# Optimization experiments

Measured on AMD Instinct MI355X. Metric: run time of the kernel, lower is better.

## Reference

```python
import jax, jax.numpy as jnp
import numpy as np

DIM = 1024
D_INNER = 2048

def setup_inputs() -> dict:
    key = jax.random.key(0)
    ks = jax.random.split(key, 8)
    B, T = 8, 1024
    x = jax.random.normal(ks[0], (B, T, DIM), dtype=jnp.float32)
    h0 = jnp.zeros((B, D_INNER), dtype=jnp.float32)
    # params (xavier-ish scales)
    in_proj_w = jax.random.normal(ks[1], (D_INNER, DIM), dtype=jnp.float32) * (2.0 / (DIM + D_INNER)) ** 0.5
    out_proj_w = jax.random.normal(ks[2], (DIM, D_INNER), dtype=jnp.float32) * (2.0 / (DIM + D_INNER)) ** 0.5
    c_h = jax.random.uniform(ks[3], (D_INNER,), jnp.float32, -0.1, 0.1)
    # spectral normalization as in _init_weights
    c_h = c_h * jnp.minimum(1.0, 0.99 / jnp.abs(jnp.fft.fft(c_h)).max())
    c_x = jax.random.uniform(ks[4], (D_INNER,), jnp.float32, -0.1, 0.1)
    c_x = c_x * jnp.minimum(1.0, 0.99 / jnp.abs(jnp.fft.fft(c_x)).max())
    b = jnp.zeros((D_INNER,), dtype=jnp.float32)
    W_gate = jax.random.normal(ks[5], (D_INNER, D_INNER), dtype=jnp.float32) * (1.0 / D_INNER) ** 0.5
    b_gate = jnp.zeros((D_INNER,), dtype=jnp.float32)
    return {"x": x, "h0": h0, "in_proj_w": in_proj_w, "out_proj_w": out_proj_w,
            "c_h": c_h, "c_x": c_x, "b": b, "W_gate": W_gate, "b_gate": b_gate}

def _circ_apply_fft(fft_c, v):
    # circ(c) @ v along last axis via real FFT; v: [..., D]
    D = v.shape[-1]
    return jnp.fft.irfft(fft_c * jnp.fft.rfft(v, axis=-1), n=D, axis=-1)

def reference(x, h0, in_proj_w, out_proj_w, c_h, c_x, b, W_gate, b_gate):
    B, T, _ = x.shape
    D = h0.shape[-1]
    x_proj = jnp.einsum('btd,ed->bte', x, in_proj_w)  # [B,T,D_inner]
    # gate path (fully parallel over T)
    gate = jax.nn.silu(jnp.einsum('bte,fe->btf', x_proj, W_gate) + b_gate)
    # input circulant contribution, parallel over all tokens
    pre = _circ_apply_fft(jnp.fft.rfft(c_x), x_proj) + b  # [B,T,D]
    fft_ch = jnp.fft.rfft(c_h)

    def step(h_prev, pre_t):
        h_new = jnp.tanh(_circ_apply_fft(fft_ch, h_prev) + pre_t)
        return h_new, h_new

    pre_tbd = jnp.transpose(pre, (1, 0, 2))  # [T,B,D]
    h_final, h_seq = jax.lax.scan(step, h0, pre_tbd)  # h_seq: [T,B,D]
    cell_out = jnp.transpose(h_seq, (1, 0, 2)) * gate  # [B,T,D]
    output = jnp.einsum('bte,de->btd', cell_out, out_proj_w)  # [B,T,dim]
    return output, h_final
```

## Files before the change

### kernel.cpp

```cpp
#include <hip/hip_runtime.h>
#include <cstdint>
#include <cstddef>

#define DI 2048
#define DM 1024
#define BB 8
#define TT 1024
#define ROWS (BB*TT)

typedef short  short8 __attribute__((ext_vector_type(8)));
typedef float  f32x4  __attribute__((ext_vector_type(4)));
typedef float  f32x16 __attribute__((ext_vector_type(16)));

__device__ __forceinline__ unsigned short f2bf(float f) {
  unsigned int u = __builtin_bit_cast(unsigned int, f);
  u = u + 0x7fffu + ((u >> 16) & 1u);
  return (unsigned short)(u >> 16);
}
__device__ __forceinline__ float fast_tanh(float x) {
  float ax = fabsf(x);
  float e  = __expf(-2.0f * ax);
  float t  = (1.0f - e) / (1.0f + e);
  return x < 0.0f ? -t : t;
}
__device__ __forceinline__ float silu_f(float z) {
  return z / (1.0f + __expf(-z));
}
__device__ __forceinline__ unsigned mulpk(unsigned a, unsigned b) {
  float a0 = __builtin_bit_cast(float, a << 16);
  float a1 = __builtin_bit_cast(float, a & 0xffff0000u);
  float b0 = __builtin_bit_cast(float, b << 16);
  float b1 = __builtin_bit_cast(float, b & 0xffff0000u);
  unsigned r0 = f2bf(a0 * b0), r1 = f2bf(a1 * b1);
  return r0 | (r1 << 16);
}
__device__ __forceinline__ uint4 pack8(const unsigned short* q) {
  uint4 p;
  p.x = (unsigned)q[0] | ((unsigned)q[1] << 16);
  p.y = (unsigned)q[2] | ((unsigned)q[3] << 16);
  p.z = (unsigned)q[4] | ((unsigned)q[5] << 16);
  p.w = (unsigned)q[6] | ((unsigned)q[7] << 16);
  return p;
}

__global__ void cast_k(const float* __restrict__ s, short* __restrict__ d, int n4) {
  int i = blockIdx.x * 256 + threadIdx.x;
  if (i >= n4) return;
  float4 f = ((const float4*)s)[i];
  unsigned lo = (unsigned)f2bf(f.x) | ((unsigned)f2bf(f.y) << 16);
  unsigned hi = (unsigned)f2bf(f.z) | ((unsigned)f2bf(f.w) << 16);
  uint2 o; o.x = lo; o.y = hi;
  ((uint2*)d)[i] = o;
}

__global__ void build_cx_k(const float* __restrict__ cx, short* __restrict__ C) {
  int tid = blockIdx.x * 256 + threadIdx.x;
  int n   = tid >> 8;
  int k0  = (tid & 255) * 8;
  unsigned short q[8];
#pragma unroll
  for (int j = 0; j < 8; ++j) q[j] = f2bf(cx[(n - (k0 + j)) & (DI - 1)]);
  *(uint4*)(C + (size_t)n * DI + k0) = pack8(q);
}

__global__ __launch_bounds__(256) void gemm_k(
    const short* __restrict__ A, const short* __restrict__ A2,
    const short* __restrict__ Bt,
    int M, int N, int K, int mode, const float* __restrict__ bias,
    float* __restrict__ outF, short* __restrict__ outH)
{
  __shared__ __align__(16) short As[128 * 40];
  __shared__ __align__(16) short Bs[128 * 40];
  const int tid  = threadIdx.x;
  const int m0   = blockIdx.y * 128, n0 = blockIdx.x * 128;
  const int wave = tid >> 6, lane = tid & 63;
  const int wy = wave >> 1, wx = wave & 1;
  const int l = lane & 15, G = lane >> 4;
  const int srow = tid >> 1, sseg = tid & 1;

  f32x4 acc[4][4];
#pragma unroll
  for (int i = 0; i < 4; ++i)
#pragma unroll
    for (int j = 0; j < 4; ++j) acc[i][j] = (f32x4){0.f, 0.f, 0.f, 0.f};

  for (int k0 = 0; k0 < K; k0 += 32) {
    if (k0) __syncthreads();
    const short* ga = A  + (size_t)(m0 + srow) * K + k0 + sseg * 16;
    const short* gb = Bt + (size_t)(n0 + srow) * K + k0 + sseg * 16;
    uint4 a0 = *(const uint4*)ga;
    uint4 a1 = *(const uint4*)(ga + 8);
    if (A2) {
      const short* g2 = A2 + (size_t)(m0 + srow) * K + k0 + sseg * 16;
      uint4 m0v = *(const uint4*)g2;
      uint4 m1v = *(const uint4*)(g2 + 8);
      a0.x = mulpk(a0.x, m0v.x); a0.y = mulpk(a0.y, m0v.y);
      a0.z = mulpk(a0.z, m0v.z); a0.w = mulpk(a0.w, m0v.w);
      a1.x = mulpk(a1.x, m1v.x); a1.y = mulpk(a1.y, m1v.y);
      a1.z = mulpk(a1.z, m1v.z); a1.w = mulpk(a1.w, m1v.w);
    }
    uint4 b0 = *(const uint4*)gb;
    uint4 b1 = *(const uint4*)(gb + 8);
    *(uint4*)&As[srow * 40 + sseg * 16]     = a0;
    *(uint4*)&As[srow * 40 + sseg * 16 + 8] = a1;
    *(uint4*)&Bs[srow * 40 + sseg * 16]     = b0;
    *(uint4*)&Bs[srow * 40 + sseg * 16 + 8] = b1;
    __syncthreads();
    short8 af[4], bfv[4];
#pragma unroll
    for (int i = 0; i < 4; ++i) af[i]  = *(const short8*)&As[(64 * wy + 16 * i + l) * 40 + 8 * G];
#pragma unroll
    for (int j = 0; j < 4; ++j) bfv[j] = *(const short8*)&Bs[(64 * wx + 16 * j + l) * 40 + 8 * G];
#pragma unroll
    for (int i = 0; i < 4; ++i)
#pragma unroll
      for (int j = 0; j < 4; ++j)
        acc[i][j] = __builtin_amdgcn_mfma_f32_16x16x32_bf16(af[i], bfv[j], acc[i][j], 0, 0, 0);
  }

#pragma unroll
  for (int j = 0; j < 4; ++j) {
    const int c = n0 + 64 * wx + 16 * j + l;
    float bv = 0.f;
    if (mode == 1 || mode == 2) bv = bias[c];
#pragma unroll
    for (int i = 0; i < 4; ++i) {
      const int r0 = m0 + 64 * wy + 16 * i + 4 * G;
#pragma unroll
      for (int v = 0; v < 4; ++v) {
        float z = acc[i][j][v] + bv;
        size_t off = (size_t)(r0 + v) * N + c;
        if (mode == 0)      outH[off] = (short)f2bf(z);
        else if (mode == 2) outH[off] = (short)f2bf(silu_f(z));
        else                outF[off] = z;
      }
    }
  }
}

__global__ __launch_bounds__(512, 2) void fused_k(
    const float* __restrict__ pre, const float* __restrict__ h0,
    const float* __restrict__ ch, short* __restrict__ hseq,
    float* __restrict__ hfin,
    const short* __restrict__ xproj, const short* __restrict__ wg,
    const float* __restrict__ bg, short* __restrict__ gate)
{
  __shared__ __align__(16) char smem[53248];
  const int bid = blockIdx.x;
  const int tid = threadIdx.x;

  if (bid < BB) {
    short* h_lds   = (short*)smem;
    float* pre_lds = (float*)(smem + 4096);
    float* part    = (float*)(smem + 20480);
    const int b = bid;
    const int wid = tid >> 6, lane = tid & 63;
    const int nh = wid & 1, kg = wid >> 1;
    const int L = lane & 31, G2 = lane >> 5;
    const int q = 32 * nh + L;
    const float* preB = pre + (size_t)b * TT * DI;

    short8 av[32];
#pragma unroll
    for (int i = 0; i < 32; ++i) {
      const int kbase = 16 * (32 * kg + i) + 8 * G2;
      short8 v;
#pragma unroll
      for (int j = 0; j < 8; ++j)
        v[j] = (short)f2bf(ch[(L - kbase - j) & (DI - 1)]);
      av[i] = v;
    }

    {
      const int n0 = 4 * tid;
      float4 hv = *(const float4*)(h0 + b * DI + n0);
      unsigned lo = (unsigned)f2bf(hv.x) | ((unsigned)f2bf(hv.y) << 16);
      unsigned hi = (unsigned)f2bf(hv.z) | ((unsigned)f2bf(hv.w) << 16);
      const int blk = tid >> 1;
      const int pblk = blk ^ ((blk >> 3) & 7);
      uint2 w; w.x = lo; w.y = hi;
      *(uint2*)&h_lds[pblk * 8 + 4 * (tid & 1)] = w;
      *(float4*)&pre_lds[n0] = *(const float4*)(preB + n0);
    }
    __syncthreads();

    const int cbase = (G2 + 4 * q + 64 * kg) & 255;

    for (int t = 0; t < TT; ++t) {
      const int cur = t & 1;
      const float* pn = preB + (size_t)(t + 1 < TT ? t + 1 : t) * DI;
      float4 pf = *(const float4*)(pn + 4 * tid);

      f32x16 acc0, acc1;
#pragma unroll
      for (int v = 0; v < 16; ++v) { acc0[v] = 0.f; acc1[v] = 0.f; }
#pragma unroll
      for (int i = 0; i < 32; i += 2) {
        int blkA = (cbase + 2 * i) & 255;
        int blkB = (cbase + 2 * i + 2) & 255;
        int pA = blkA ^ ((blkA >> 3) & 7);
        int pB = blkB ^ ((blkB >> 3) & 7);
        short8 bvA = *(const short8*)&h_lds[pA * 8];
        short8 bvB = *(const short8*)&h_lds[pB * 8];
        acc0 = __builtin_amdgcn_mfma_f32_32x32x16_bf16(av[i],     bvA, acc0, 0, 0, 0);
        acc1 = __builtin_amdgcn_mfma_f32_32x32x16_bf16(av[i + 1], bvB, acc1, 0, 0, 0);
      }
      {
        float* pk = part + kg * DI;
#pragma unroll
        for (int s = 0; s < 4; ++s) {
          const int blk4 = 2 * s + G2 + 8 * q;
          const int p4 = blk4 ^ ((blk4 >> 3) & 7);
          float4 w;
          w.x = acc0[4 * s + 0] + acc1[4 * s + 0];
          w.y = acc0[4 * s + 1] + acc1[4 * s + 1];
          w.z = acc0[4 * s + 2] + acc1[4 * s + 2];
          w.w = acc0[4 * s + 3] + acc1[4 * s + 3];
          *(float4*)&pk[4 * p4] = w;
        }
        *(float4*)&pre_lds[(cur ^ 1) * DI + 4 * tid] = pf;
      }
      __syncthreads();
      {
        const int pb = tid ^ ((tid >> 3) & 7);
        float4 c0 = *(const float4*)&part[4 * pb];
        float4 c1 = *(const float4*)&part[DI + 4 * pb];
        float4 c2 = *(const float4*)&part[2 * DI + 4 * pb];
        float4 c3 = *(const float4*)&part[3 * DI + 4 * pb];
        float4 pr = *(const float4*)&pre_lds[cur * DI + 4 * tid];
        float z0 = c0.x + c1.x + c2.x + c3.x + pr.x;
        float z1 = c0.y + c1.y + c2.y + c3.y + pr.y;
        float z2 = c0.z + c1.z + c2.z + c3.z + pr.z;
        float z3 = c0.w + c1.w + c2.w + c3.w + pr.w;
        float t0 = fast_tanh(z0), t1 = fast_tanh(z1);
        float t2 = fast_tanh(z2), t3 = fast_tanh(z3);
        unsigned lo = (unsigned)f2bf(t0) | ((unsigned)f2bf(t1) << 16);
        unsigned hi = (unsigned)f2bf(t2) | ((unsigned)f2bf(t3) << 16);
        const int blk = tid >> 1;
        const int pblk = blk ^ ((blk >> 3) & 7);
        uint2 w; w.x = lo; w.y = hi;
        *(uint2*)&h_lds[pblk * 8 + 4 * (tid & 1)] = w;
        *(uint2*)(hseq + (size_t)(b * TT + t) * DI + 4 * tid) = w;
        if (t == TT - 1) {
          float4 hf; hf.x = t0; hf.y = t1; hf.z = t2; hf.w = t3;
          *(float4*)(hfin + b * DI + 4 * tid) = hf;
        }
      }
      __syncthreads();
    }
  } else {
    short* As = (short*)smem;
    short* Bs = (short*)(smem + 20480);
    const int wid = tid >> 6, lane = tid & 63;
    const int wy = wid >> 1, wx = wid & 1;
    const int l = lane & 15, G = lane >> 4;

    for (int tile = bid - BB; tile < 512; tile += 248) {
      const int m0 = (tile & 31) * 256, n0 = (tile >> 5) * 128;
      f32x4 acc[4][4];
#pragma unroll
      for (int i = 0; i < 4; ++i)
#pragma unroll
        for (int j = 0; j < 4; ++j) acc[i][j] = (f32x4){0.f, 0.f, 0.f, 0.f};

      for (int k0 = 0; k0 < DI; k0 += 32) {
        __syncthreads();
        const short* ga = xproj + (size_t)(m0 + (tid >> 1)) * DI + k0 + (tid & 1) * 16;
        const short* gb = wg    + (size_t)(n0 + (tid >> 2)) * DI + k0 + (tid & 3) * 8;
        uint4 a0 = *(const uint4*)ga;
        uint4 a1 = *(const uint4*)(ga + 8);
        uint4 b0 = *(const uint4*)gb;
        *(uint4*)&As[(tid >> 1) * 40 + (tid & 1) * 16]     = a0;
        *(uint4*)&As[(tid >> 1) * 40 + (tid & 1) * 16 + 8] = a1;
        *(uint4*)&Bs[(tid >> 2) * 40 + (tid & 3) * 8]      = b0;
        __syncthreads();
        short8 af[4], bfv[4];
#pragma unroll
        for (int i = 0; i < 4; ++i) af[i]  = *(const short8*)&As[(64 * wy + 16 * i + l) * 40 + 8 * G];
#pragma unroll
        for (int j = 0; j < 4; ++j) bfv[j] = *(const short8*)&Bs[(64 * wx + 16 * j + l) * 40 + 8 * G];
#pragma unroll
        for (int i = 0; i < 4; ++i)
#pragma unroll
          for (int j = 0; j < 4; ++j)
            acc[i][j] = __builtin_amdgcn_mfma_f32_16x16x32_bf16(af[i], bfv[j], acc[i][j], 0, 0, 0);
      }
#pragma unroll
      for (int j = 0; j < 4; ++j) {
        const int c = n0 + 64 * wx + 16 * j + l;
        const float bv = bg[c];
#pragma unroll
        for (int i = 0; i < 4; ++i) {
          const int r0 = m0 + 64 * wy + 16 * i + 4 * G;
#pragma unroll
          for (int v = 0; v < 4; ++v) {
            float z = acc[i][j][v] + bv;
            gate[(size_t)(r0 + v) * DI + c] = (short)f2bf(silu_f(z));
          }
        }
      }
      __syncthreads();
    }
  }
}

extern "C" void kernel_launch(void* const* d_in, const int* in_sizes, int n_in,
                              void* d_out, int out_size, void* d_ws, size_t ws_size,
                              hipStream_t stream) {
  const float* x    = (const float*)d_in[0];
  const float* h0   = (const float*)d_in[1];
  const float* win  = (const float*)d_in[2];
  const float* wout = (const float*)d_in[3];
  const float* ch   = (const float*)d_in[4];
  const float* cx   = (const float*)d_in[5];
  const float* bb   = (const float*)d_in[6];
  const float* wg   = (const float*)d_in[7];
  const float* bg   = (const float*)d_in[8];
  float* out = (float*)d_out;

  char* ws = (char*)d_ws;
  short* o_xb    = (short*)(ws + 0);
  short* o_win   = (short*)(ws + 16777216);
  short* o_cx    = (short*)(ws + 20971520);
  short* o_hseq  = (short*)(ws + 0);
  short* o_xproj = (short*)(ws + 33554432);
  float* o_pre   = (float*)(ws + 67108864);
  short* o_wout  = (short*)(ws + 67108864);
  short* o_gate  = (short*)(ws + 134217728);
  short* o_wg    = (short*)(ws + 167772160);

  cast_k<<<8192, 256, 0, stream>>>(x,   o_xb,  (BB * TT * DM) / 4);
  cast_k<<<2048, 256, 0, stream>>>(win, o_win, (DI * DM) / 4);
  cast_k<<<4096, 256, 0, stream>>>(wg,  o_wg,  (DI * DI) / 4);
  build_cx_k<<<2048, 256, 0, stream>>>(cx, o_cx);

  gemm_k<<<dim3(DI / 128, ROWS / 128), 256, 0, stream>>>(
      o_xb, nullptr, o_win, ROWS, DI, DM, 0, nullptr, nullptr, o_xproj);

  gemm_k<<<dim3(DI / 128, ROWS / 128), 256, 0, stream>>>(
      o_xproj, nullptr, o_cx, ROWS, DI, DI, 1, bb, o_pre, nullptr);

  fused_k<<<256, 512, 0, stream>>>(o_pre, h0, ch, o_hseq,
                                   out + (size_t)BB * TT * DM,
                                   o_xproj, o_wg, bg, o_gate);

  cast_k<<<2048, 256, 0, stream>>>(wout, o_wout, (DM * DI) / 4);

  gemm_k<<<dim3(DM / 128, ROWS / 128), 256, 0, stream>>>(
      o_hseq, o_gate, o_wout, ROWS, DM, DI, 3, nullptr, out, nullptr);
}
```

Baseline: 2.145 ms.

## Repartition recurrent matvec across 8 K-groups with dual-row-tile reuse

The recurrent circulant matvec now splits work over 8 K-groups, one per wave, instead of 2 row halves by 4 K-groups. Each wave computes both 32-row output tiles and reuses every loaded h fragment for two MFMAs, halving the LDS reads of h per MFMA. It also keeps the next step's pre value in a register instead of double-buffering it through LDS. The cost is 8 partial-sum buffers, which raises LDS to 69632 bytes and makes the final reduction wider. More accumulator registers are live, which may hurt occupancy for the co-resident GEMM blocks.

```diff
diff --git a/kernel.cpp b/kernel.cpp
--- a/kernel.cpp
+++ b/kernel.cpp
@@ -145,93 +145,100 @@
     const short* __restrict__ xproj, const short* __restrict__ wg,
     const float* __restrict__ bg, short* __restrict__ gate)
 {
-  __shared__ __align__(16) char smem[53248];
+  __shared__ __align__(16) char smem[69632];
   const int bid = blockIdx.x;
   const int tid = threadIdx.x;
 
   if (bid < BB) {
-    short* h_lds   = (short*)smem;
-    float* pre_lds = (float*)(smem + 4096);
-    float* part    = (float*)(smem + 20480);
+    short* h_lds = (short*)smem;
+    float* part  = (float*)(smem + 4096);
     const int b = bid;
-    const int wid = tid >> 6, lane = tid & 63;
-    const int nh = wid & 1, kg = wid >> 1;
+    const int kg = tid >> 6;
+    const int lane = tid & 63;
     const int L = lane & 31, G2 = lane >> 5;
-    const int q = 32 * nh + L;
     const float* preB = pre + (size_t)b * TT * DI;
 
-    short8 av[32];
-#pragma unroll
-    for (int i = 0; i < 32; ++i) {
-      const int kbase = 16 * (32 * kg + i) + 8 * G2;
-      short8 v;
-#pragma unroll
-      for (int j = 0; j < 8; ++j)
-        v[j] = (short)f2bf(ch[(L - kbase - j) & (DI - 1)]);
-      av[i] = v;
+    short8 av0[16], av1[16];
+#pragma unroll
+    for (int i = 0; i < 16; ++i) {
+      const int kb = 256 * kg + 16 * i + 8 * G2;
+      short8 v0, v1;
+#pragma unroll
+      for (int j = 0; j < 8; ++j) {
+        v0[j] = (short)f2bf(ch[(L - kb - j) & (DI - 1)]);
+        v1[j] = (short)f2bf(ch[(L + 32 - kb - j) & (DI - 1)]);
+      }
+      av0[i] = v0; av1[i] = v1;
     }
 
     {
-      const int n0 = 4 * tid;
-      float4 hv = *(const float4*)(h0 + b * DI + n0);
+      float4 hv = *(const float4*)(h0 + b * DI + 4 * tid);
       unsigned lo = (unsigned)f2bf(hv.x) | ((unsigned)f2bf(hv.y) << 16);
       unsigned hi = (unsigned)f2bf(hv.z) | ((unsigned)f2bf(hv.w) << 16);
       const int blk = tid >> 1;
       const int pblk = blk ^ ((blk >> 3) & 7);
       uint2 w; w.x = lo; w.y = hi;
       *(uint2*)&h_lds[pblk * 8 + 4 * (tid & 1)] = w;
-      *(float4*)&pre_lds[n0] = *(const float4*)(preB + n0);
-    }
+    }
+    float4 pcur = *(const float4*)(preB + 4 * tid);
     __syncthreads();
 
-    const int cbase = (G2 + 4 * q + 64 * kg) & 255;
+    const int cb = 32 * kg + G2 + 8 * L;
+    const int pt = tid ^ ((tid >> 4) & 7);
 
     for (int t = 0; t < TT; ++t) {
-      const int cur = t & 1;
-      const float* pn = preB + (size_t)(t + 1 < TT ? t + 1 : t) * DI;
-      float4 pf = *(const float4*)(pn + 4 * tid);
-
-      f32x16 acc0, acc1;
-#pragma unroll
-      for (int v = 0; v < 16; ++v) { acc0[v] = 0.f; acc1[v] = 0.f; }
-#pragma unroll
-      for (int i = 0; i < 32; i += 2) {
-        int blkA = (cbase + 2 * i) & 255;
-        int blkB = (cbase + 2 * i + 2) & 255;
-        int pA = blkA ^ ((blkA >> 3) & 7);
-        int pB = blkB ^ ((blkB >> 3) & 7);
-        short8 bvA = *(const short8*)&h_lds[pA * 8];
-        short8 bvB = *(const short8*)&h_lds[pB * 8];
-        acc0 = __builtin_amdgcn_mfma_f32_32x32x16_bf16(av[i],     bvA, acc0, 0, 0, 0);
-        acc1 = __builtin_amdgcn_mfma_f32_32x32x16_bf16(av[i + 1], bvB, acc1, 0, 0, 0);
+      float4 pf = *(const float4*)(preB + (size_t)(t + 1 < TT ? t + 1 : t) * DI + 4 * tid);
+
+      f32x16 a0a, a0b, a1a, a1b;
+#pragma unroll
+      for (int v = 0; v < 16; ++v) { a0a[v] = 0.f; a0b[v] = 0.f; a1a[v] = 0.f; a1b[v] = 0.f; }
+#pragma unroll
+      for (int i = 0; i < 16; i += 2) {
+        int b0 = (cb + 2 * i) & 255;       b0 ^= (b0 >> 3) & 7;
+        int b1 = (cb + 2 * i + 2) & 255;   b1 ^= (b1 >> 3) & 7;
+        short8 bv0 = *(const short8*)&h_lds[b0 * 8];
+        short8 bv1 = *(const short8*)&h_lds[b1 * 8];
+        a0a = __builtin_amdgcn_mfma_f32_32x32x16_bf16(av0[i],     bv0, a0a, 0, 0, 0);
+        a1a = __builtin_amdgcn_mfma_f32_32x32x16_bf16(av1[i],     bv0, a1a, 0, 0, 0);
+        a0b = __builtin_amdgcn_mfma_f32_32x32x16_bf16(av0[i + 1], bv1, a0b, 0, 0, 0);
+        a1b = __builtin_amdgcn_mfma_f32_32x32x16_bf16(av1[i + 1], bv1, a1b, 0, 0, 0);
       }
       {
         float* pk = part + kg * DI;
 #pragma unroll
         for (int s = 0; s < 4; ++s) {
-          const int blk4 = 2 * s + G2 + 8 * q;
-          const int p4 = blk4 ^ ((blk4 >> 3) & 7);
-          float4 w;
-          w.x = acc0[4 * s + 0] + acc1[4 * s + 0];
-          w.y = acc0[4 * s + 1] + acc1[4 * s + 1];
-          w.z = acc0[4 * s + 2] + acc1[4 * s + 2];
-          w.w = acc0[4 * s + 3] + acc1[4 * s + 3];
-          *(float4*)&pk[4 * p4] = w;
+          int b40 = 2 * s + G2 + 16 * L;
+          int p40 = b40 ^ ((b40 >> 4) & 7);
+          float4 w0;
+          w0.x = a0a[4 * s + 0] + a0b[4 * s + 0];
+          w0.y = a0a[4 * s + 1] + a0b[4 * s + 1];
+          w0.z = a0a[4 * s + 2] + a0b[4 * s + 2];
+          w0.w = a0a[4 * s + 3] + a0b[4 * s + 3];
+          *(float4*)&pk[4 * p40] = w0;
+          int b41 = b40 + 8;
+          int p41 = b41 ^ ((b41 >> 4) & 7);
+          float4 w1;
+          w1.x = a1a[4 * s + 0] + a1b[4 * s + 0];
+          w1.y = a1a[4 * s + 1] + a1b[4 * s + 1];
+          w1.z = a1a[4 * s + 2] + a1b[4 * s + 2];
+          w1.w = a1a[4 * s + 3] + a1b[4 * s + 3];
+          *(float4*)&pk[4 * p41] = w1;
         }
-        *(float4*)&pre_lds[(cur ^ 1) * DI + 4 * tid] = pf;
       }
       __syncthreads();
       {
-        const int pb = tid ^ ((tid >> 3) & 7);
-        float4 c0 = *(const float4*)&part[4 * pb];
-        float4 c1 = *(const float4*)&part[DI + 4 * pb];
-        float4 c2 = *(const float4*)&part[2 * DI + 4 * pb];
-        float4 c3 = *(const float4*)&part[3 * DI + 4 * pb];
-        float4 pr = *(const float4*)&pre_lds[cur * DI + 4 * tid];
-        float z0 = c0.x + c1.x + c2.x + c3.x + pr.x;
-        float z1 = c0.y + c1.y + c2.y + c3.y + pr.y;
-        float z2 = c0.z + c1.z + c2.z + c3.z + pr.z;
-        float z3 = c0.w + c1.w + c2.w + c3.w + pr.w;
+        float4 c0 = *(const float4*)&part[0 * DI + 4 * pt];
+        float4 c1 = *(const float4*)&part[1 * DI + 4 * pt];
+        float4 c2 = *(const float4*)&part[2 * DI + 4 * pt];
+        float4 c3 = *(const float4*)&part[3 * DI + 4 * pt];
+        float4 c4 = *(const float4*)&part[4 * DI + 4 * pt];
+        float4 c5 = *(const float4*)&part[5 * DI + 4 * pt];
+        float4 c6 = *(const float4*)&part[6 * DI + 4 * pt];
+        float4 c7 = *(const float4*)&part[7 * DI + 4 * pt];
+        float z0 = ((c0.x + c1.x) + (c2.x + c3.x)) + ((c4.x + c5.x) + (c6.x + c7.x)) + pcur.x;
+        float z1 = ((c0.y + c1.y) + (c2.y + c3.y)) + ((c4.y + c5.y) + (c6.y + c7.y)) + pcur.y;
+        float z2 = ((c0.z + c1.z) + (c2.z + c3.z)) + ((c4.z + c5.z) + (c6.z + c7.z)) + pcur.z;
+        float z3 = ((c0.w + c1.w) + (c2.w + c3.w)) + ((c4.w + c5.w) + (c6.w + c7.w)) + pcur.w;
         float t0 = fast_tanh(z0), t1 = fast_tanh(z1);
         float t2 = fast_tanh(z2), t3 = fast_tanh(z3);
         unsigned lo = (unsigned)f2bf(t0) | ((unsigned)f2bf(t1) << 16);
@@ -247,6 +254,7 @@
         }
       }
       __syncthreads();
+      pcur = pf;
     }
   } else {
     short* As = (short*)smem;
```

New measurement: 2.299 ms. 7.1% more time.

## Restructure recurrence step: register-held pre, 4 MFMA chains, deferred hseq store

Applied to the files above, without the earlier changes.

The recurrent blocks now keep the next timestep's pre values in registers instead of staging them through a double-buffered LDS array, which cuts the shared-memory footprint. The work is remapped so each wave covers a 32-row half of a 512-wide k-group and runs four independent MFMA accumulator chains instead of two, giving more latency hiding in the serial step. The global store of h for step t is moved to the start of step t+1 so it overlaps the next step's compute. The cost is more accumulator registers and a new LDS swizzle for the partial sums.

```diff
diff --git a/kernel.cpp b/kernel.cpp
--- a/kernel.cpp
+++ b/kernel.cpp
@@ -145,109 +145,110 @@
     const short* __restrict__ xproj, const short* __restrict__ wg,
     const float* __restrict__ bg, short* __restrict__ gate)
 {
-  __shared__ __align__(16) char smem[53248];
+  __shared__ __align__(16) char smem[36864];
   const int bid = blockIdx.x;
   const int tid = threadIdx.x;
 
   if (bid < BB) {
-    short* h_lds   = (short*)smem;
-    float* pre_lds = (float*)(smem + 4096);
-    float* part    = (float*)(smem + 20480);
+    short* h_lds = (short*)smem;
+    float* part  = (float*)(smem + 4096);
     const int b = bid;
     const int wid = tid >> 6, lane = tid & 63;
-    const int nh = wid & 1, kg = wid >> 1;
+    const int kg = wid & 3, mh = wid >> 2;
     const int L = lane & 31, G2 = lane >> 5;
-    const int q = 32 * nh + L;
     const float* preB = pre + (size_t)b * TT * DI;
 
     short8 av[32];
 #pragma unroll
     for (int i = 0; i < 32; ++i) {
-      const int kbase = 16 * (32 * kg + i) + 8 * G2;
+      const int kb = 512 * kg + 16 * i + 8 * G2;
+      const int row = L + 32 * mh;
       short8 v;
 #pragma unroll
       for (int j = 0; j < 8; ++j)
-        v[j] = (short)f2bf(ch[(L - kbase - j) & (DI - 1)]);
+        v[j] = (short)f2bf(ch[(row - kb - j) & (DI - 1)]);
       av[i] = v;
     }
 
     {
-      const int n0 = 4 * tid;
-      float4 hv = *(const float4*)(h0 + b * DI + n0);
+      float4 hv = *(const float4*)(h0 + b * DI + 4 * tid);
       unsigned lo = (unsigned)f2bf(hv.x) | ((unsigned)f2bf(hv.y) << 16);
       unsigned hi = (unsigned)f2bf(hv.z) | ((unsigned)f2bf(hv.w) << 16);
       const int blk = tid >> 1;
       const int pblk = blk ^ ((blk >> 3) & 7);
       uint2 w; w.x = lo; w.y = hi;
       *(uint2*)&h_lds[pblk * 8 + 4 * (tid & 1)] = w;
-      *(float4*)&pre_lds[n0] = *(const float4*)(preB + n0);
-    }
+    }
+    float4 pcur = *(const float4*)(preB + 4 * tid);
     __syncthreads();
 
-    const int cbase = (G2 + 4 * q + 64 * kg) & 255;
+    const int cb = 64 * kg + G2 + 8 * L;
+    const int pt4 = tid ^ ((tid >> 4) & 7);
+    uint2 hw;
 
     for (int t = 0; t < TT; ++t) {
-      const int cur = t & 1;
-      const float* pn = preB + (size_t)(t + 1 < TT ? t + 1 : t) * DI;
-      float4 pf = *(const float4*)(pn + 4 * tid);
-
-      f32x16 acc0, acc1;
-#pragma unroll
-      for (int v = 0; v < 16; ++v) { acc0[v] = 0.f; acc1[v] = 0.f; }
-#pragma unroll
-      for (int i = 0; i < 32; i += 2) {
-        int blkA = (cbase + 2 * i) & 255;
-        int blkB = (cbase + 2 * i + 2) & 255;
-        int pA = blkA ^ ((blkA >> 3) & 7);
-        int pB = blkB ^ ((blkB >> 3) & 7);
-        short8 bvA = *(const short8*)&h_lds[pA * 8];
-        short8 bvB = *(const short8*)&h_lds[pB * 8];
-        acc0 = __builtin_amdgcn_mfma_f32_32x32x16_bf16(av[i],     bvA, acc0, 0, 0, 0);
-        acc1 = __builtin_amdgcn_mfma_f32_32x32x16_bf16(av[i + 1], bvB, acc1, 0, 0, 0);
+      if (t > 0)
+        *(uint2*)(hseq + (size_t)(b * TT + t - 1) * DI + 4 * tid) = hw;
+      float4 pf = *(const float4*)(preB + (size_t)(t + 1 < TT ? t + 1 : t) * DI + 4 * tid);
+
+      f32x16 ac0, ac1, ac2, ac3;
+#pragma unroll
+      for (int v = 0; v < 16; ++v) { ac0[v] = 0.f; ac1[v] = 0.f; ac2[v] = 0.f; ac3[v] = 0.f; }
+#pragma unroll
+      for (int i = 0; i < 32; i += 4) {
+        int b0 = (cb + 2 * i) & 255;       b0 ^= (b0 >> 3) & 7;
+        int b1 = (cb + 2 * i + 2) & 255;   b1 ^= (b1 >> 3) & 7;
+        int b2 = (cb + 2 * i + 4) & 255;   b2 ^= (b2 >> 3) & 7;
+        int b3 = (cb + 2 * i + 6) & 255;   b3 ^= (b3 >> 3) & 7;
+        short8 bv0 = *(const short8*)&h_lds[b0 * 8];
+        short8 bv1 = *(const short8*)&h_lds[b1 * 8];
+        short8 bv2 = *(const short8*)&h_lds[b2 * 8];
+        short8 bv3 = *(const short8*)&h_lds[b3 * 8];
+        ac0 = __builtin_amdgcn_mfma_f32_32x32x16_bf16(av[i],     bv0, ac0, 0, 0, 0);
+        ac1 = __builtin_amdgcn_mfma_f32_32x32x16_bf16(av[i + 1], bv1, ac1, 0, 0, 0);
+        ac2 = __builtin_amdgcn_mfma_f32_32x32x16_bf16(av[i + 2], bv2, ac2, 0, 0, 0);
+        ac3 = __builtin_amdgcn_mfma_f32_32x32x16_bf16(av[i + 3], bv3, ac3, 0, 0, 0);
       }
       {
         float* pk = part + kg * DI;
 #pragma unroll
         for (int s = 0; s < 4; ++s) {
-          const int blk4 = 2 * s + G2 + 8 * q;
-          const int p4 = blk4 ^ ((blk4 >> 3) & 7);
+          int b4 = 2 * s + G2 + 8 * mh + 16 * L;
+          int p4 = b4 ^ ((b4 >> 4) & 7);
           float4 w;
-          w.x = acc0[4 * s + 0] + acc1[4 * s + 0];
-          w.y = acc0[4 * s + 1] + acc1[4 * s + 1];
-          w.z = acc0[4 * s + 2] + acc1[4 * s + 2];
-          w.w = acc0[4 * s + 3] + acc1[4 * s + 3];
+          w.x = (ac0[4 * s + 0] + ac1[4 * s + 0]) + (ac2[4 * s + 0] + ac3[4 * s + 0]);
+          w.y = (ac0[4 * s + 1] + ac1[4 * s + 1]) + (ac2[4 * s + 1] + ac3[4 * s + 1]);
+          w.z = (ac0[4 * s + 2] + ac1[4 * s + 2]) + (ac2[4 * s + 2] + ac3[4 * s + 2]);
+          w.w = (ac0[4 * s + 3] + ac1[4 * s + 3]) + (ac2[4 * s + 3] + ac3[4 * s + 3]);
           *(float4*)&pk[4 * p4] = w;
         }
-        *(float4*)&pre_lds[(cur ^ 1) * DI + 4 * tid] = pf;
       }
       __syncthreads();
       {
-        const int pb = tid ^ ((tid >> 3) & 7);
-        float4 c0 = *(const float4*)&part[4 * pb];
-        float4 c1 = *(const float4*)&part[DI + 4 * pb];
-        float4 c2 = *(const float4*)&part[2 * DI + 4 * pb];
-        float4 c3 = *(const float4*)&part[3 * DI + 4 * pb];
-        float4 pr = *(const float4*)&pre_lds[cur * DI + 4 * tid];
-        float z0 = c0.x + c1.x + c2.x + c3.x + pr.x;
-        float z1 = c0.y + c1.y + c2.y + c3.y + pr.y;
-        float z2 = c0.z + c1.z + c2.z + c3.z + pr.z;
-        float z3 = c0.w + c1.w + c2.w + c3.w + pr.w;
+        float4 c0 = *(const float4*)&part[0 * DI + 4 * pt4];
+        float4 c1 = *(const float4*)&part[1 * DI + 4 * pt4];
+        float4 c2 = *(const float4*)&part[2 * DI + 4 * pt4];
+        float4 c3 = *(const float4*)&part[3 * DI + 4 * pt4];
+        float z0 = (c0.x + c1.x) + (c2.x + c3.x) + pcur.x;
+        float z1 = (c0.y + c1.y) + (c2.y + c3.y) + pcur.y;
+        float z2 = (c0.z + c1.z) + (c2.z + c3.z) + pcur.z;
+        float z3 = (c0.w + c1.w) + (c2.w + c3.w) + pcur.w;
         float t0 = fast_tanh(z0), t1 = fast_tanh(z1);
         float t2 = fast_tanh(z2), t3 = fast_tanh(z3);
-        unsigned lo = (unsigned)f2bf(t0) | ((unsigned)f2bf(t1) << 16);
-        unsigned hi = (unsigned)f2bf(t2) | ((unsigned)f2bf(t3) << 16);
+        hw.x = (unsigned)f2bf(t0) | ((unsigned)f2bf(t1) << 16);
+        hw.y = (unsigned)f2bf(t2) | ((unsigned)f2bf(t3) << 16);
         const int blk = tid >> 1;
         const int pblk = blk ^ ((blk >> 3) & 7);
-        uint2 w; w.x = lo; w.y = hi;
-        *(uint2*)&h_lds[pblk * 8 + 4 * (tid & 1)] = w;
-        *(uint2*)(hseq + (size_t)(b * TT + t) * DI + 4 * tid) = w;
+        *(uint2*)&h_lds[pblk * 8 + 4 * (tid & 1)] = hw;
         if (t == TT - 1) {
           float4 hf; hf.x = t0; hf.y = t1; hf.z = t2; hf.w = t3;
           *(float4*)(hfin + b * DI + 4 * tid) = hf;
         }
       }
       __syncthreads();
-    }
+      pcur = pf;
+    }
+    *(uint2*)(hseq + (size_t)(b * TT + TT - 1) * DI + 4 * tid) = hw;
   } else {
     short* As = (short*)smem;
     short* Bs = (short*)(smem + 20480);
```

New measurement: 2.441 ms. 13.8% more time.

## Load GEMM tiles directly to LDS and defer hseq store in scan loop

Applied to the files above, without the earlier changes.

In the generic GEMM, tile loads for B (and A when there is no multiplier) go straight from global memory into LDS with global_load_lds, replacing the register round trip. The padding of the LDS rows is dropped to fit the direct-load layout, which may bring back bank conflicts on the fragment reads. In the recurrent scan, the bf16 hidden-state store to hseq moves to the start of the next timestep so the global write sits off the tail of the critical step. The last step is written after the loop.

```diff
diff --git a/kernel.cpp b/kernel.cpp
--- a/kernel.cpp
+++ b/kernel.cpp
@@ -11,6 +11,9 @@
 typedef short  short8 __attribute__((ext_vector_type(8)));
 typedef float  f32x4  __attribute__((ext_vector_type(4)));
 typedef float  f32x16 __attribute__((ext_vector_type(16)));
+
+typedef __attribute__((address_space(1))) const void gvoid;
+typedef __attribute__((address_space(3))) void svoid;
 
 __device__ __forceinline__ unsigned short f2bf(float f) {
   unsigned int u = __builtin_bit_cast(unsigned int, f);
@@ -69,14 +72,14 @@
     int M, int N, int K, int mode, const float* __restrict__ bias,
     float* __restrict__ outF, short* __restrict__ outH)
 {
-  __shared__ __align__(16) short As[128 * 40];
-  __shared__ __align__(16) short Bs[128 * 40];
+  __shared__ __align__(16) short As[128 * 32];
+  __shared__ __align__(16) short Bs[128 * 32];
   const int tid  = threadIdx.x;
   const int m0   = blockIdx.y * 128, n0 = blockIdx.x * 128;
   const int wave = tid >> 6, lane = tid & 63;
   const int wy = wave >> 1, wx = wave & 1;
   const int l = lane & 15, G = lane >> 4;
-  const int srow = tid >> 1, sseg = tid & 1;
+  const int row = tid >> 2, seg = (tid & 3) * 8;
 
   f32x4 acc[4][4];
 #pragma unroll
@@ -85,32 +88,39 @@
     for (int j = 0; j < 4; ++j) acc[i][j] = (f32x4){0.f, 0.f, 0.f, 0.f};
 
   for (int k0 = 0; k0 < K; k0 += 32) {
-    if (k0) __syncthreads();
-    const short* ga = A  + (size_t)(m0 + srow) * K + k0 + sseg * 16;
-    const short* gb = Bt + (size_t)(n0 + srow) * K + k0 + sseg * 16;
-    uint4 a0 = *(const uint4*)ga;
-    uint4 a1 = *(const uint4*)(ga + 8);
+    __syncthreads();
     if (A2) {
+      const int srow = tid >> 1, sseg = tid & 1;
+      const short* ga = A  + (size_t)(m0 + srow) * K + k0 + sseg * 16;
       const short* g2 = A2 + (size_t)(m0 + srow) * K + k0 + sseg * 16;
+      uint4 a0 = *(const uint4*)ga;
+      uint4 a1 = *(const uint4*)(ga + 8);
       uint4 m0v = *(const uint4*)g2;
       uint4 m1v = *(const uint4*)(g2 + 8);
       a0.x = mulpk(a0.x, m0v.x); a0.y = mulpk(a0.y, m0v.y);
       a0.z = mulpk(a0.z, m0v.z); a0.w = mulpk(a0.w, m0v.w);
       a1.x = mulpk(a1.x, m1v.x); a1.y = mulpk(a1.y, m1v.y);
       a1.z = mulpk(a1.z, m1v.z); a1.w = mulpk(a1.w, m1v.w);
-    }
-    uint4 b0 = *(const uint4*)gb;
-    uint4 b1 = *(const uint4*)(gb + 8);
-    *(uint4*)&As[srow * 40 + sseg * 16]     = a0;
-    *(uint4*)&As[srow * 40 + sseg * 16 + 8] = a1;
-    *(uint4*)&Bs[srow * 40 + sseg * 16]     = b0;
-    *(uint4*)&Bs[srow * 40 + sseg * 16 + 8] = b1;
+      *(uint4*)&As[srow * 32 + sseg * 16]     = a0;
+      *(uint4*)&As[srow * 32 + sseg * 16 + 8] = a1;
+    } else {
+      const short* ga0 = A + (size_t)(m0 + row) * K + k0 + seg;
+      const short* ga1 = A + (size_t)(m0 + 64 + row) * K + k0 + seg;
+      __builtin_amdgcn_global_load_lds((gvoid*)ga0, (svoid*)(As + wave * 512),        16, 0, 0);
+      __builtin_amdgcn_global_load_lds((gvoid*)ga1, (svoid*)(As + 2048 + wave * 512), 16, 0, 0);
+    }
+    {
+      const short* gb0 = Bt + (size_t)(n0 + row) * K + k0 + seg;
+      const short* gb1 = Bt + (size_t)(n0 + 64 + row) * K + k0 + seg;
+      __builtin_amdgcn_global_load_lds((gvoid*)gb0, (svoid*)(Bs + wave * 512),        16, 0, 0);
+      __builtin_amdgcn_global_load_lds((gvoid*)gb1, (svoid*)(Bs + 2048 + wave * 512), 16, 0, 0);
+    }
     __syncthreads();
     short8 af[4], bfv[4];
 #pragma unroll
-    for (int i = 0; i < 4; ++i) af[i]  = *(const short8*)&As[(64 * wy + 16 * i + l) * 40 + 8 * G];
-#pragma unroll
-    for (int j = 0; j < 4; ++j) bfv[j] = *(const short8*)&Bs[(64 * wx + 16 * j + l) * 40 + 8 * G];
+    for (int i = 0; i < 4; ++i) af[i]  = *(const short8*)&As[(64 * wy + 16 * i + l) * 32 + 8 * G];
+#pragma unroll
+    for (int j = 0; j < 4; ++j) bfv[j] = *(const short8*)&Bs[(64 * wx + 16 * j + l) * 32 + 8 * G];
 #pragma unroll
     for (int i = 0; i < 4; ++i)
 #pragma unroll
@@ -185,9 +195,12 @@
     __syncthreads();
 
     const int cbase = (G2 + 4 * q + 64 * kg) & 255;
+    uint2 hw;
 
     for (int t = 0; t < TT; ++t) {
       const int cur = t & 1;
+      if (t > 0)
+        *(uint2*)(hseq + (size_t)(b * TT + t - 1) * DI + 4 * tid) = hw;
       const float* pn = preB + (size_t)(t + 1 < TT ? t + 1 : t) * DI;
       float4 pf = *(const float4*)(pn + 4 * tid);
 
@@ -234,13 +247,11 @@
         float z3 = c0.w + c1.w + c2.w + c3.w + pr.w;
         float t0 = fast_tanh(z0), t1 = fast_tanh(z1);
         float t2 = fast_tanh(z2), t3 = fast_tanh(z3);
-        unsigned lo = (unsigned)f2bf(t0) | ((unsigned)f2bf(t1) << 16);
-        unsigned hi = (unsigned)f2bf(t2) | ((unsigned)f2bf(t3) << 16);
+        hw.x = (unsigned)f2bf(t0) | ((unsigned)f2bf(t1) << 16);
+        hw.y = (unsigned)f2bf(t2) | ((unsigned)f2bf(t3) << 16);
         const int blk = tid >> 1;
         const int pblk = blk ^ ((blk >> 3) & 7);
-        uint2 w; w.x = lo; w.y = hi;
-        *(uint2*)&h_lds[pblk * 8 + 4 * (tid & 1)] = w;
-        *(uint2*)(hseq + (size_t)(b * TT + t) * DI + 4 * tid) = w;
+        *(uint2*)&h_lds[pblk * 8 + 4 * (tid & 1)] = hw;
         if (t == TT - 1) {
           float4 hf; hf.x = t0; hf.y = t1; hf.z = t2; hf.w = t3;
           *(float4*)(hfin + b * DI + 4 * tid) = hf;
@@ -248,6 +259,7 @@
       }
       __syncthreads();
     }
+    *(uint2*)(hseq + (size_t)(b * TT + TT - 1) * DI + 4 * tid) = hw;
   } else {
     short* As = (short*)smem;
     short* Bs = (short*)(smem + 20480);
```

Measured after the change: 2.274 ms. 6.0% more time.
